# Kernel optimization log

Hardware: AMD Instinct MI355X
Metric: run time of the kernel (lower is better)

## Reference

```python
import jax, jax.numpy as jnp
import numpy as np

B, C_IN, HW, N = 128, 1024, 14, 196
D_MODEL, NH, HD, DFF = 384, 12, 32, 1536
ALPHA, BETA, GAMMA = 1.9, 3.8, 15.2
BETA_INT = int(BETA)          # 3
S = 2 * BETA_INT + 1          # 7
NUM_BUCKETS = S * S           # 49
BN_EPS = 2e-5


def _piecewise_index(d):
    # iRPE piecewise index (numpy, static): linear inside |d|<=alpha, log outside
    ad = np.abs(d).astype(np.float64)
    y = np.sign(d) * np.minimum(
        np.round(ALPHA + np.log(np.maximum(ad, ALPHA) / ALPHA) / np.log(GAMMA / ALPHA) * (BETA - ALPHA)),
        BETA)
    return np.where(ad <= ALPHA, d, y).astype(np.int64)  # trunc toward zero like torch .to(int)


def _make_rp_bucket():
    coords = np.stack(np.meshgrid(np.arange(HW), np.arange(HW), indexing='ij'), -1).reshape(-1, 2)
    diff = coords[:, None, :] - coords[None, :, :]  # [N,N,2]
    r = _piecewise_index(diff[..., 0]) + BETA_INT   # [0, 2*beta_int]
    c = _piecewise_index(diff[..., 1]) + BETA_INT
    return (r * S + c).astype(np.int32)            # [N,N] in [0,49)


RP_BUCKET = jnp.asarray(_make_rp_bucket())  # [196,196] int32, static


def _ln(x, w, b, eps=1e-5):
    mu = x.mean(-1, keepdims=True)
    var = ((x - mu) ** 2).mean(-1, keepdims=True)
    return (x - mu) * jax.lax.rsqrt(var + eps) * w + b


def setup_inputs() -> dict:
    key = jax.random.key(0)
    ks = jax.random.split(key, 12)
    g = lambda i, shape, s=0.02: jax.random.normal(ks[i], shape, jnp.float32) * s
    return {
        'x': jax.random.normal(ks[0], (B, C_IN, HW, HW), jnp.float32),
        'embed_fc1_w': g(1, (1024, C_IN)), 'embed_fc1_b': jnp.zeros((1024,), jnp.float32),
        'embed_fc2_w': g(2, (D_MODEL, 1024)), 'embed_fc2_b': jnp.zeros((D_MODEL,), jnp.float32),
        'pos_conv_w': g(3, (D_MODEL, 1, 3, 3), 0.1), 'pos_conv_b': jnp.zeros((D_MODEL,), jnp.float32),
        'ln1_w': jnp.ones((D_MODEL,), jnp.float32), 'ln1_b': jnp.zeros((D_MODEL,), jnp.float32),
        'qkv_w': g(4, (3 * D_MODEL, D_MODEL)),
        'rpe_table': g(5, (HD, NUM_BUCKETS)),
        'proj_w': g(6, (D_MODEL, D_MODEL)), 'proj_b': jnp.zeros((D_MODEL,), jnp.float32),
        'ln2_w': jnp.ones((D_MODEL,), jnp.float32), 'ln2_b': jnp.zeros((D_MODEL,), jnp.float32),
        'mlp_fc1_w': g(7, (DFF, D_MODEL)), 'mlp_fc1_b': jnp.zeros((DFF,), jnp.float32),
        'mlp_fc2_w': g(8, (D_MODEL, DFF)), 'mlp_fc2_b': jnp.zeros((D_MODEL,), jnp.float32),
        'bn1_w': jnp.ones((N,), jnp.float32), 'bn1_b': jnp.zeros((N,), jnp.float32),
        'lin_w': g(9, (D_MODEL, D_MODEL * N)), 'lin_b': jnp.zeros((D_MODEL,), jnp.float32),
        'bn2_w': jnp.ones((D_MODEL,), jnp.float32), 'bn2_b': jnp.zeros((D_MODEL,), jnp.float32),
    }


def reference(x, embed_fc1_w, embed_fc1_b, embed_fc2_w, embed_fc2_b,
              pos_conv_w, pos_conv_b, ln1_w, ln1_b, qkv_w, rpe_table,
              proj_w, proj_b, ln2_w, ln2_b, mlp_fc1_w, mlp_fc1_b,
              mlp_fc2_w, mlp_fc2_b, bn1_w, bn1_b, lin_w, lin_b, bn2_w, bn2_b):
    b = x.shape[0]
    # --- EmbedMLP: [B,C,14,14] -> [B,196,C] -> relu6 MLP -> [B,196,384]
    t = x.reshape(b, C_IN, N).transpose(0, 2, 1)
    t = jnp.clip(t @ embed_fc1_w.T + embed_fc1_b, 0.0, 6.0)
    t = t @ embed_fc2_w.T + embed_fc2_b
    # --- PosCNN: depthwise 3x3 conv + residual
    img = t.transpose(0, 2, 1).reshape(b, D_MODEL, HW, HW)
    conv = jax.lax.conv_general_dilated(
        img, pos_conv_w, (1, 1), 'SAME',
        dimension_numbers=('NCHW', 'OIHW', 'NCHW'), feature_group_count=D_MODEL)
    img = conv + pos_conv_b[None, :, None, None] + img
    t = img.reshape(b, D_MODEL, N).transpose(0, 2, 1)  # [B,196,384]
    # --- Attention with iRPE-on-k bias
    h = _ln(t, ln1_w, ln1_b)
    qkv = (h @ qkv_w.T).reshape(b, N, 3, NH, HD).transpose(2, 0, 3, 1, 4)
    scale = HD ** -0.5
    q = qkv[0] * scale
    k = qkv[1]
    v = qkv[2]
    attn = jnp.einsum('bhid,bhjd->bhij', q, k)
    # ctx-mode shared-head rpe_k: bias[b,h,i,j] = sum_d q[b,h,i,d] * table[d, bucket[i,j]]
    rpe_scores = jnp.einsum('bhid,dn->bhin', q, rpe_table)        # [B,H,N,49]
    bias = rpe_scores[:, :, jnp.arange(N)[:, None], RP_BUCKET]     # [B,H,N,N]
    attn = jax.nn.softmax(attn + bias, axis=-1)
    out = jnp.einsum('bhij,bhjd->bhid', attn, v)
    out = out.transpose(0, 2, 1, 3).reshape(b, N, D_MODEL)
    t = t + (out @ proj_w.T + proj_b)
    # --- MLP block
    h = _ln(t, ln2_w, ln2_b)
    h = jnp.clip(h @ mlp_fc1_w.T + mlp_fc1_b, 0.0, 6.0)
    t = t + (h @ mlp_fc2_w.T + mlp_fc2_b)
    # --- BatchNorm1d(196) over dims (batch, feature) per token channel (train-mode stats)
    mu = t.mean(axis=(0, 2), keepdims=True)
    var = t.var(axis=(0, 2), keepdims=True)
    t = (t - mu) * jax.lax.rsqrt(var + BN_EPS) * bn1_w[None, :, None] + bn1_b[None, :, None]
    # --- Flatten + Linear(196*384 -> 384)
    y = t.reshape(b, N * D_MODEL) @ lin_w.T + lin_b
    # --- BatchNorm1d(384) over batch (train-mode stats)
    mu2 = y.mean(axis=0, keepdims=True)
    var2 = y.var(axis=0, keepdims=True)
    y = (y - mu2) * jax.lax.rsqrt(var2 + BN_EPS) * bn2_w + bn2_b
    return y
```

## Files before the change

### kernel.cpp

```cpp
#include <hip/hip_runtime.h>
#include <cstdint>

#define B_    128
#define CIN   1024
#define NPOS  196
#define DM    384
#define NH_   12
#define HD_   32
#define DFF_  1536
#define MT    25088
#define SCALE_Q 0.17677669529663687f

typedef unsigned short u16;
typedef __attribute__((ext_vector_type(8))) short  short8;
typedef __attribute__((ext_vector_type(4))) float  f32x4;

__device__ __forceinline__ u16 f2bf(float f) {
  union { float f; uint32_t u; } v; v.f = f;
  uint32_t u = v.u;
  return (u16)((u + 0x7fffu + ((u >> 16) & 1u)) >> 16);
}
__device__ __forceinline__ float bf2f(u16 h) {
  union { uint32_t u; float f; } v; v.u = ((uint32_t)h) << 16;
  return v.f;
}

#define GLDS16(g, l)                                                           \
  __builtin_amdgcn_global_load_lds(                                            \
      (const __attribute__((address_space(1))) void*)(g),                      \
      (__attribute__((address_space(3))) void*)(l), 16, 0, 0)

template <int MODE>
__global__ __launch_bounds__(256) void gemm_k(
    const u16* __restrict__ A, const void* __restrict__ Wv,
    const float* __restrict__ bias, const float* __restrict__ res,
    void* __restrict__ outp,
    int M, int N, int K, int lda, int ldw, int nTN, int splitK)
{
  __shared__ __align__(16) u16 As[2][4 * 128 * 8];
  __shared__ __align__(16) u16 Bs[2][4 * 128 * 8];

  int nwg = gridDim.x;
  int bid0 = blockIdx.x;
  int qq = nwg >> 3, rr = nwg & 7;
  int xcd = bid0 & 7, idx = bid0 >> 3;
  int bid = (xcd < rr ? xcd * (qq + 1) : rr * (qq + 1) + (xcd - rr) * qq) + idx;

  int split = 0, mT, nT;
  if (MODE == 4) { split = bid / nTN; nT = bid % nTN; mT = 0; }
  else           { mT = bid / nTN;    nT = bid % nTN; }

  const u16* Ab = A + (size_t)split * splitK;
  float* outF = (float*)outp + ((MODE == 4) ? (size_t)split * (size_t)M * N : (size_t)0);
  u16*   outU = (u16*)outp;

  int tid = threadIdx.x;
  int wv = tid >> 6, ln = tid & 63;
  int q = ln >> 4, c = ln & 15;
  int wr = wv >> 1, wc = wv & 1;
  int mBase = mT * 128, nBase = nT * 128;

  f32x4 acc[4][4];
#pragma unroll
  for (int i = 0; i < 4; i++)
#pragma unroll
    for (int j = 0; j < 4; j++) acc[i][j] = (f32x4){0.f, 0.f, 0.f, 0.f};

  const u16* Ag = Ab + (size_t)mBase * lda;
  const u16*  Wg16 = (const u16*)Wv + (size_t)split * splitK + (size_t)nBase * ldw;
  const float* Wg32 = (const float*)Wv + (size_t)split * splitK + (size_t)nBase * ldw;

  int sl = ln & 3, rsub = ln >> 2;

  short8 ra[2], rb16[2];
  float4 rbf[2][2];

  auto LOADREG = [&](int t) {
    int k0 = t * 32;
#pragma unroll
    for (int i = 0; i < 2; i++) {
      int r = wv * 32 + i * 16 + rsub;
      ra[i] = *(const short8*)(Ag + (size_t)r * lda + k0 + sl * 8);
      if constexpr (MODE == 4) {
        const float* wp = Wg32 + (size_t)r * ldw + k0 + sl * 8;
        rbf[i][0] = *(const float4*)wp;
        rbf[i][1] = *(const float4*)(wp + 4);
      } else {
        rb16[i] = *(const short8*)(Wg16 + (size_t)r * ldw + k0 + sl * 8);
      }
    }
  };
  auto WRITE = [&](int buf) {
#pragma unroll
    for (int i = 0; i < 2; i++) {
      int r = wv * 32 + i * 16 + rsub;
      *(short8*)&As[buf][(sl * 128 + r) * 8] = ra[i];
      if constexpr (MODE == 4) {
        short8 pk;
        pk[0] = (short)f2bf(rbf[i][0].x); pk[1] = (short)f2bf(rbf[i][0].y);
        pk[2] = (short)f2bf(rbf[i][0].z); pk[3] = (short)f2bf(rbf[i][0].w);
        pk[4] = (short)f2bf(rbf[i][1].x); pk[5] = (short)f2bf(rbf[i][1].y);
        pk[6] = (short)f2bf(rbf[i][1].z); pk[7] = (short)f2bf(rbf[i][1].w);
        *(short8*)&Bs[buf][(sl * 128 + r) * 8] = pk;
      } else {
        *(short8*)&Bs[buf][(sl * 128 + r) * 8] = rb16[i];
      }
    }
  };

  int NT = K >> 5;

  LOADREG(0);
  WRITE(0);
  if (NT > 1) LOADREG(1);
  asm volatile("s_waitcnt lgkmcnt(0)" ::: "memory");
  __builtin_amdgcn_s_barrier();

  int cur = 0;
  for (int t = 0; t < NT; ++t) {
    if (t + 1 < NT) WRITE(cur ^ 1);
    short8 afr[4], bfr[4];
#pragma unroll
    for (int mt2 = 0; mt2 < 4; mt2++)
      afr[mt2] = *(const short8*)&As[cur][((q * 128) + wr * 64 + mt2 * 16 + c) * 8];
#pragma unroll
    for (int nt2 = 0; nt2 < 4; nt2++)
      bfr[nt2] = *(const short8*)&Bs[cur][((q * 128) + wc * 64 + nt2 * 16 + c) * 8];
    if (t + 2 < NT) LOADREG(t + 2);
    __builtin_amdgcn_sched_barrier(0);
#pragma unroll
    for (int mt2 = 0; mt2 < 4; mt2++)
#pragma unroll
      for (int nt2 = 0; nt2 < 4; nt2++)
        acc[mt2][nt2] = __builtin_amdgcn_mfma_f32_16x16x32_bf16(
            afr[mt2], bfr[nt2], acc[mt2][nt2], 0, 0, 0);
    asm volatile("s_waitcnt lgkmcnt(0)" ::: "memory");
    __builtin_amdgcn_s_barrier();
    cur ^= 1;
  }

#pragma unroll
  for (int mt2 = 0; mt2 < 4; mt2++) {
    int row0 = mBase + wr * 64 + mt2 * 16 + q * 4;
#pragma unroll
    for (int nt2 = 0; nt2 < 4; nt2++) {
      int col = nBase + wc * 64 + nt2 * 16 + c;
      float bv = (MODE == 0 || MODE == 1 || MODE == 3) ? bias[col] : 0.f;
      f32x4 v = acc[mt2][nt2];
#pragma unroll
      for (int e = 0; e < 4; e++) {
        int row = row0 + e;
        float x = v[e] + bv;
        if (MODE == 0) x = fminf(fmaxf(x, 0.f), 6.f);
        if (MODE == 3) x += res[(size_t)row * N + col];
        if (MODE == 0 || MODE == 2) outU[(size_t)row * N + col] = f2bf(x);
        else                        outF[(size_t)row * N + col] = x;
      }
    }
  }
}

__global__ __launch_bounds__(224) void blut_k(uint8_t* __restrict__ lut)
{
  int i = blockIdx.x;
  int j = threadIdx.x;
  uint8_t v = 49;
  if (j < 196) {
    int ri = i / 14, ci = i - ri * 14;
    int rj = j / 14, cj = j - rj * 14;
    int dr = ri - rj, dc = ci - cj;
    int adr = dr < 0 ? -dr : dr, adc = dc < 0 ? -dc : dc;
    int tr = adr <= 1 ? adr : (adr <= 3 ? 2 : 3);
    int tc = adc <= 1 ? adc : (adc <= 3 ? 2 : 3);
    int fr = dr < 0 ? -tr : tr, fc = dc < 0 ? -tc : tc;
    v = (uint8_t)(fr * 7 + fc + 24);
  }
  lut[i * 224 + j] = v;
}

__global__ __launch_bounds__(256) void attn_k(
    const u16* __restrict__ QKV, const float* __restrict__ tabG,
    const uint8_t* __restrict__ lutG, u16* __restrict__ AO)
{
  __shared__ __align__(16) u16 Ks[4 * 196 * 8];
  __shared__ __align__(16) u16 Vt[32 * 228];
  __shared__ __align__(16) u16 Pc4[4][2][512];
  __shared__ __align__(16) u16 Ts[49 * 32];
  __shared__ __align__(16) u16 Rw4[4][2][16 * 50];
  int bh = blockIdx.x; int b = bh / NH_, h = bh % NH_;
  int tid = threadIdx.x;
  int wv = tid >> 6, ln = tid & 63;
  int q = ln >> 4, c = ln & 15;
  size_t rowbase = (size_t)b * NPOS * 1152 + h * 32;

  for (int cb = wv * 64; cb < 784; cb += 256) {
    int ch = cb + ln;
    if (ch < 784) {
      int s = ch / 196, j = ch - s * 196;
      GLDS16(QKV + rowbase + 384 + (size_t)j * 1152 + s * 8, &Ks[cb * 8]);
    }
  }
  for (int t = tid; t < 49 * 32; t += 256) {
    int tt = t >> 5, k = t & 31;
    Ts[t] = f2bf(tabG[k * 49 + tt]);
  }
  for (int t = tid; t < 784; t += 256) {
    int nn = t >> 2, d0 = (t & 3) * 8;
    short8 v = *(const short8*)(QKV + rowbase + 768 + (size_t)nn * 1152 + d0);
#pragma unroll
    for (int j = 0; j < 8; j++) Vt[(d0 + j) * 228 + nn] = (u16)v[j];
  }
  for (int t = tid; t < 32 * 32; t += 256) {
    int d = t >> 5, jj = 196 + (t & 31);
    Vt[d * 228 + jj] = 0;
  }
  __syncthreads();

  for (int it = 0; it < 2; ++it) {
    int mtA = wv + it * 8;
    bool vB = (mtA + 4) < 13;
    int mbx[2];
    mbx[0] = mtA * 16;
    mbx[1] = (vB ? (mtA + 4) : 12) * 16;

    short8 afrag[2];
    int i0x[2], lutOff[2][4];
#pragma unroll
    for (int x = 0; x < 2; x++) {
      int irow = mbx[x] + c; if (irow > 195) irow = 195;
      afrag[x] = *(const short8*)(QKV + rowbase + (size_t)irow * 1152 + q * 8);
      i0x[x] = mbx[x] + q * 4;
#pragma unroll
      for (int e = 0; e < 4; e++) {
        int i = i0x[x] + e; if (i > 195) i = 195;
        lutOff[x][e] = i * 224;
      }
    }
    int rwOff[4];
#pragma unroll
    for (int e = 0; e < 4; e++) rwOff[e] = (q * 4 + e) * 50;

#pragma unroll
    for (int nt = 0; nt < 4; nt++) {
      int t = nt * 16 + c;
      int tt = t < 49 ? t : 48;
      short8 tb = *(const short8*)&Ts[tt * 32 + q * 8];
#pragma unroll
      for (int x = 0; x < 2; x++) {
        f32x4 z = {0.f, 0.f, 0.f, 0.f};
        f32x4 rr = __builtin_amdgcn_mfma_f32_16x16x32_bf16(afrag[x], tb, z, 0, 0, 0);
        if (t < 49) {
#pragma unroll
          for (int e = 0; e < 4; e++)
            Rw4[wv][x][rwOff[e] + t] = f2bf(rr[e] * SCALE_Q);
        }
      }
    }
    if (c == 0) {
#pragma unroll
      for (int x = 0; x < 2; x++)
#pragma unroll
        for (int e = 0; e < 4; e++)
          Rw4[wv][x][rwOff[e] + 49] = 0xFF80;
    }

    float mr[2] = {-INFINITY, -INFINITY};
    float l4[2][4] = {{0.f,0.f,0.f,0.f},{0.f,0.f,0.f,0.f}};
    f32x4 oacc[2][2];
#pragma unroll
    for (int x = 0; x < 2; x++) {
      oacc[x][0] = (f32x4){0.f, 0.f, 0.f, 0.f};
      oacc[x][1] = (f32x4){0.f, 0.f, 0.f, 0.f};
    }

    for (int ck = 0; ck < 7; ck++) {
      short8 bfr[2];
#pragma unroll
      for (int t = 0; t < 2; t++) {
        int j = (ck * 2 + t) * 16 + c;
        int jc = j > 195 ? 195 : j;
        bfr[t] = *(const short8*)&Ks[(q * 196 + jc) * 8];
      }
      f32x4 s01[2][2];
#pragma unroll
      for (int x = 0; x < 2; x++) {
        f32x4 z = {0.f, 0.f, 0.f, 0.f};
        s01[x][0] = __builtin_amdgcn_mfma_f32_16x16x32_bf16(afrag[x], bfr[0], z, 0, 0, 0);
        s01[x][1] = __builtin_amdgcn_mfma_f32_16x16x32_bf16(afrag[x], bfr[1], z, 0, 0, 0);
      }
      uint8_t bk[2][2][4];
#pragma unroll
      for (int t = 0; t < 2; t++) {
        int jj = ck * 32 + t * 16 + c;
#pragma unroll
        for (int x = 0; x < 2; x++)
#pragma unroll
          for (int e = 0; e < 4; e++) bk[x][t][e] = lutG[lutOff[x][e] + jj];
      }
#pragma unroll
      for (int x = 0; x < 2; x++)
#pragma unroll
        for (int t = 0; t < 2; t++)
#pragma unroll
          for (int e = 0; e < 4; e++)
            s01[x][t][e] = s01[x][t][e] * SCALE_Q + bf2f(Rw4[wv][x][rwOff[e] + bk[x][t][e]]);

#pragma unroll
      for (int x = 0; x < 2; x++) {
        float mc = s01[x][0][0];
#pragma unroll
        for (int t = 0; t < 2; t++)
#pragma unroll
          for (int e = 0; e < 4; e++) mc = fmaxf(mc, s01[x][t][e]);
#pragma unroll
        for (int o = 1; o < 16; o <<= 1) mc = fmaxf(mc, __shfl_xor(mc, o, 64));
        float mn = fmaxf(mr[x], mc);
        float sc = __expf(mr[x] - mn);
        mr[x] = mn;
#pragma unroll
        for (int t = 0; t < 2; t++)
#pragma unroll
          for (int e = 0; e < 4; e++) s01[x][t][e] = __expf(s01[x][t][e] - mn);
#pragma unroll
        for (int e = 0; e < 4; e++) {
          l4[x][e] = l4[x][e] * sc + s01[x][0][e] + s01[x][1][e];
          oacc[x][0][e] *= sc; oacc[x][1][e] *= sc;
        }
#pragma unroll
        for (int t = 0; t < 2; t++) {
          int sl2 = t * 2 + (c >> 3);
#pragma unroll
          for (int e = 0; e < 4; e++) {
            union { float f; uint32_t u; } pv; pv.f = s01[x][t][e];
            Pc4[wv][x][(sl2 * 16 + q * 4 + e) * 8 + (c & 7)] = (u16)(pv.u >> 16);
          }
        }
      }
#pragma unroll
      for (int n2 = 0; n2 < 2; n2++) {
        short8 vb = *(const short8*)&Vt[(n2 * 16 + c) * 228 + ck * 32 + q * 8];
#pragma unroll
        for (int x = 0; x < 2; x++) {
          short8 pa = *(const short8*)&Pc4[wv][x][(q * 16 + c) * 8];
          oacc[x][n2] = __builtin_amdgcn_mfma_f32_16x16x32_bf16(pa, vb, oacc[x][n2], 0, 0, 0);
        }
      }
    }

#pragma unroll
    for (int x = 0; x < 2; x++) {
      if (x == 1 && !vB) continue;
      float inv[4];
#pragma unroll
      for (int e = 0; e < 4; e++) {
        float s2 = l4[x][e];
#pragma unroll
        for (int o = 1; o < 16; o <<= 1) s2 += __shfl_xor(s2, o, 64);
        inv[e] = 1.f / s2;
      }
#pragma unroll
      for (int n2 = 0; n2 < 2; n2++) {
#pragma unroll
        for (int e = 0; e < 4; e++) {
          int i = i0x[x] + e;
          if (i < 196) {
            int d = n2 * 16 + c;
            AO[((size_t)b * NPOS + i) * DM + h * 32 + d] = f2bf(oacc[x][n2][e] * inv[e]);
          }
        }
      }
    }
  }
}

__global__ __launch_bounds__(256) void transpose_cast_k(
    const float* __restrict__ x, u16* __restrict__ At)
{
  __shared__ float t[32][33];
  int c0 = blockIdx.x * 32, n0 = blockIdx.y * 32, b = blockIdx.z;
  int tx = threadIdx.x, ty = threadIdx.y;
  const float* xb = x + (size_t)b * CIN * NPOS;
#pragma unroll
  for (int i = 0; i < 4; i++) {
    int cc = c0 + ty + i * 8, nn = n0 + tx;
    t[ty + i * 8][tx] = (nn < NPOS) ? xb[(size_t)cc * NPOS + nn] : 0.f;
  }
  __syncthreads();
  u16* Ab = At + (size_t)b * NPOS * CIN;
#pragma unroll
  for (int i = 0; i < 4; i++) {
    int nn = n0 + ty + i * 8, cc = c0 + tx;
    if (nn < NPOS) Ab[(size_t)nn * CIN + cc] = f2bf(t[tx][ty + i * 8]);
  }
}

__global__ __launch_bounds__(256) void conv_res_k(
    const float* __restrict__ T0, const float* __restrict__ pcw,
    const float* __restrict__ pcb, float* __restrict__ T1)
{
  int idx = blockIdx.x * 256 + threadIdx.x;
  if (idx >= B_ * NPOS * 96) return;
  int d4 = idx % 96; int rem = idx / 96;
  int n = rem % NPOS; int b = rem / NPOS;
  int hh = n / 14, ww = n % 14;
  int d0 = d4 * 4;
  float w9[4][9];
#pragma unroll
  for (int j = 0; j < 4; j++)
#pragma unroll
    for (int t = 0; t < 9; t++) w9[j][t] = pcw[(d0 + j) * 9 + t];
  const float* base = T0 + (size_t)b * NPOS * DM;
  float4 ctr = *(const float4*)(base + (size_t)n * DM + d0);
  float ax = ctr.x + pcb[d0], ay = ctr.y + pcb[d0 + 1];
  float az = ctr.z + pcb[d0 + 2], aw = ctr.w + pcb[d0 + 3];
#pragma unroll
  for (int kh = 0; kh < 3; kh++) {
    int h2 = hh + kh - 1;
    if (h2 < 0 || h2 >= 14) continue;
#pragma unroll
    for (int kw = 0; kw < 3; kw++) {
      int w2 = ww + kw - 1;
      if (w2 < 0 || w2 >= 14) continue;
      float4 v = *(const float4*)(base + (size_t)(h2 * 14 + w2) * DM + d0);
      int t = kh * 3 + kw;
      ax += v.x * w9[0][t]; ay += v.y * w9[1][t];
      az += v.z * w9[2][t]; aw += v.w * w9[3][t];
    }
  }
  float4 o = {ax, ay, az, aw};
  *(float4*)(T1 + (size_t)b * NPOS * DM + (size_t)n * DM + d0) = o;
}

__global__ __launch_bounds__(256) void ln_k(
    const float* __restrict__ in, const float* __restrict__ w,
    const float* __restrict__ bb, u16* __restrict__ out)
{
  int row = blockIdx.x * 4 + (threadIdx.x >> 6);
  int ln = threadIdx.x & 63;
  const float2* r = (const float2*)(in + (size_t)row * DM);
  float2 v[3]; float s = 0.f, sq = 0.f;
#pragma unroll
  for (int j = 0; j < 3; j++) {
    v[j] = r[ln + 64 * j];
    s += v[j].x + v[j].y; sq += v[j].x * v[j].x + v[j].y * v[j].y;
  }
#pragma unroll
  for (int o = 1; o < 64; o <<= 1) { s += __shfl_xor(s, o, 64); sq += __shfl_xor(sq, o, 64); }
  float mu = s * (1.f / 384.f);
  float var = sq * (1.f / 384.f) - mu * mu;
  float rs = rsqrtf(var + 1e-5f);
  uint32_t* orow = (uint32_t*)(out + (size_t)row * DM);
#pragma unroll
  for (int j = 0; j < 3; j++) {
    int d = (ln + 64 * j) * 2;
    float a = (v[j].x - mu) * rs * w[d] + bb[d];
    float bq = (v[j].y - mu) * rs * w[d + 1] + bb[d + 1];
    orow[ln + 64 * j] = (uint32_t)f2bf(a) | ((uint32_t)f2bf(bq) << 16);
  }
}

__global__ __launch_bounds__(256) void bn1_partial_k(
    const float* __restrict__ T3, float* __restrict__ part)
{
  int n = blockIdx.x >> 3, g = blockIdx.x & 7;
  int tid = threadIdx.x;
  float s = 0.f, sq = 0.f;
  for (int b2 = g * 16; b2 < g * 16 + 16; b2++) {
    const float* p = T3 + ((size_t)b2 * NPOS + n) * DM;
    for (int d = tid; d < DM; d += 256) { float v = p[d]; s += v; sq += v * v; }
  }
#pragma unroll
  for (int o = 1; o < 64; o <<= 1) { s += __shfl_xor(s, o, 64); sq += __shfl_xor(sq, o, 64); }
  __shared__ float ls[4], lq[4];
  int wv = tid >> 6, ln = tid & 63;
  if (ln == 0) { ls[wv] = s; lq[wv] = sq; }
  __syncthreads();
  if (tid == 0) {
    part[blockIdx.x * 2]     = ls[0] + ls[1] + ls[2] + ls[3];
    part[blockIdx.x * 2 + 1] = lq[0] + lq[1] + lq[2] + lq[3];
  }
}

__global__ __launch_bounds__(256) void bn1_finish_k(
    const float* __restrict__ part, const float* __restrict__ bw,
    const float* __restrict__ bbb, float* __restrict__ scaleArr,
    float* __restrict__ shiftArr)
{
  int n = threadIdx.x;
  if (n >= NPOS) return;
  float S = 0.f, Q = 0.f;
#pragma unroll
  for (int g = 0; g < 8; g++) { S += part[(n * 8 + g) * 2]; Q += part[(n * 8 + g) * 2 + 1]; }
  float mu = S / 49152.f;
  float var = Q / 49152.f - mu * mu;
  float rs = rsqrtf(var + 2e-5f);
  float sc = rs * bw[n];
  scaleArr[n] = sc;
  shiftArr[n] = bbb[n] - mu * sc;
}

__global__ __launch_bounds__(256) void bn1_apply_k(
    const float* __restrict__ T3, const float* __restrict__ scaleArr,
    const float* __restrict__ shiftArr, u16* __restrict__ outb)
{
  int idx = blockIdx.x * 256 + threadIdx.x;
  if (idx >= MT * DM / 4) return;
  int n = (idx / 96) % NPOS;
  float4 v = *(const float4*)(T3 + (size_t)idx * 4);
  float sc = scaleArr[n], sh = shiftArr[n];
  uint32_t p0 = (uint32_t)f2bf(v.x * sc + sh) | ((uint32_t)f2bf(v.y * sc + sh) << 16);
  uint32_t p1 = (uint32_t)f2bf(v.z * sc + sh) | ((uint32_t)f2bf(v.w * sc + sh) << 16);
  ((uint2*)outb)[idx] = make_uint2(p0, p1);
}

__global__ __launch_bounds__(256) void lin_reduce_k(
    const float* __restrict__ part, const float* __restrict__ lb,
    float* __restrict__ y)
{
  int idx = blockIdx.x * 256 + threadIdx.x;
  if (idx >= 128 * DM) return;
  int col = idx % DM;
  float s = lb[col];
#pragma unroll
  for (int sp = 0; sp < 49; sp++) s += part[(size_t)sp * (128 * DM) + idx];
  y[idx] = s;
}

__global__ __launch_bounds__(64) void bn2_k(
    float* __restrict__ y, const float* __restrict__ w,
    const float* __restrict__ bb)
{
  int col = blockIdx.x; int ln = threadIdx.x;
  float v0 = y[(size_t)ln * DM + col];
  float v1 = y[(size_t)(ln + 64) * DM + col];
  float s = v0 + v1, sq = v0 * v0 + v1 * v1;
#pragma unroll
  for (int o = 1; o < 64; o <<= 1) { s += __shfl_xor(s, o, 64); sq += __shfl_xor(sq, o, 64); }
  float mu = s / 128.f;
  float var = sq / 128.f - mu * mu;
  float rs = rsqrtf(var + 2e-5f);
  float sc = rs * w[col], sh = bb[col] - mu * sc;
  y[(size_t)ln * DM + col] = v0 * sc + sh;
  y[(size_t)(ln + 64) * DM + col] = v1 * sc + sh;
}

__global__ __launch_bounds__(256) void castall_k(
    const float* __restrict__ s0, u16* __restrict__ d0,
    const float* __restrict__ s1, u16* __restrict__ d1,
    const float* __restrict__ s2, u16* __restrict__ d2,
    const float* __restrict__ s3, u16* __restrict__ d3,
    const float* __restrict__ s4, u16* __restrict__ d4,
    const float* __restrict__ s5, u16* __restrict__ d5)
{
  const int b0 = 262144, b1 = b0 + 98304, b2 = b1 + 110592,
            b3 = b2 + 36864, b4 = b3 + 147456, b5 = b4 + 147456;
  int idx = blockIdx.x * 256 + threadIdx.x;
  int stride = gridDim.x * 256;
  for (; idx < b5; idx += stride) {
    const float* s; u16* d; int l;
    if      (idx < b0) { s = s0; d = d0; l = idx; }
    else if (idx < b1) { s = s1; d = d1; l = idx - b0; }
    else if (idx < b2) { s = s2; d = d2; l = idx - b1; }
    else if (idx < b3) { s = s3; d = d3; l = idx - b2; }
    else if (idx < b4) { s = s4; d = d4; l = idx - b3; }
    else               { s = s5; d = d5; l = idx - b4; }
    float4 v = *(const float4*)(s + (size_t)l * 4);
    uint32_t p0 = (uint32_t)f2bf(v.x) | ((uint32_t)f2bf(v.y) << 16);
    uint32_t p1 = (uint32_t)f2bf(v.z) | ((uint32_t)f2bf(v.w) << 16);
    ((uint2*)d)[l] = make_uint2(p0, p1);
  }
}

extern "C" void kernel_launch(void* const* d_in, const int* in_sizes, int n_in,
                              void* d_out, int out_size, void* d_ws, size_t ws_size,
                              hipStream_t stream)
{
  (void)in_sizes; (void)n_in; (void)out_size;
  const float* x    = (const float*)d_in[0];
  const float* fc1w = (const float*)d_in[1];
  const float* fc1b = (const float*)d_in[2];
  const float* fc2w = (const float*)d_in[3];
  const float* fc2b = (const float*)d_in[4];
  const float* pcw  = (const float*)d_in[5];
  const float* pcb  = (const float*)d_in[6];
  const float* ln1w = (const float*)d_in[7];
  const float* ln1b = (const float*)d_in[8];
  const float* qkvw = (const float*)d_in[9];
  const float* rpet = (const float*)d_in[10];
  const float* projw= (const float*)d_in[11];
  const float* projb= (const float*)d_in[12];
  const float* ln2w = (const float*)d_in[13];
  const float* ln2b = (const float*)d_in[14];
  const float* m1w  = (const float*)d_in[15];
  const float* m1b  = (const float*)d_in[16];
  const float* m2w  = (const float*)d_in[17];
  const float* m2b  = (const float*)d_in[18];
  const float* bn1w = (const float*)d_in[19];
  const float* bn1b = (const float*)d_in[20];
  const float* linw = (const float*)d_in[21];
  const float* linb = (const float*)d_in[22];
  const float* bn2w = (const float*)d_in[23];
  const float* bn2b = (const float*)d_in[24];
  float* y = (float*)d_out;

  const size_t RA = 0;
  const size_t RB = 77070336;
  const size_t RC = RB + 57802752;
  const size_t RD = RC + 19267584;
  const size_t RE = RD + 38535168;
  const size_t RF = RE + 38535168;
  const size_t RG = RF + 9633792;
  const size_t RS = RG + 6422528;
  const size_t NEED = RS + 2048 + 16384 + 45056;
  if (ws_size < NEED) return;

  char* ws = (char*)d_ws;
  u16*   At    = (u16*)(ws + RA);
  u16*   MLP1  = (u16*)(ws + RA);
  u16*   U     = (u16*)(ws + RB);
  u16*   QKV   = (u16*)(ws + RB);
  u16*   T3nb  = (u16*)(ws + RB);
  u16*   H     = (u16*)(ws + RC);
  u16*   AO    = (u16*)(ws + RC);
  u16*   H2    = (u16*)(ws + RC);
  float* T0    = (float*)(ws + RD);
  float* T2    = (float*)(ws + RD);
  float* T1    = (float*)(ws + RE);
  float* T3    = (float*)(ws + RE);
  float* PART  = (float*)(ws + RF);
  u16*   wb_fc1 = (u16*)(ws + RG);
  u16*   wb_fc2 = wb_fc1 + 1048576;
  u16*   wb_qkv = wb_fc2 + 393216;
  u16*   wb_proj= wb_qkv + 442368;
  u16*   wb_m1  = wb_proj + 147456;
  u16*   wb_m2  = wb_m1 + 589824;
  float* bnS   = (float*)(ws + RS);
  float* bnSh  = bnS + 196;
  float* bnP   = (float*)(ws + RS + 2048);
  uint8_t* blut = (uint8_t*)(ws + RS + 2048 + 16384);

  castall_k<<<1024, 256, 0, stream>>>(fc1w, wb_fc1, fc2w, wb_fc2, qkvw, wb_qkv,
                                      projw, wb_proj, m1w, wb_m1, m2w, wb_m2);
  blut_k<<<196, 224, 0, stream>>>(blut);

  transpose_cast_k<<<dim3(32, 7, 128), dim3(32, 8), 0, stream>>>(x, At);

  gemm_k<0><<<196 * 8, 256, 0, stream>>>(At, wb_fc1, fc1b, nullptr, U,
                                          MT, 1024, 1024, 1024, 1024, 8, 0);
  gemm_k<1><<<196 * 3, 256, 0, stream>>>(U, wb_fc2, fc2b, nullptr, T0,
                                          MT, 384, 1024, 1024, 1024, 3, 0);
  conv_res_k<<<(B_ * NPOS * 96 + 255) / 256, 256, 0, stream>>>(T0, pcw, pcb, T1);
  ln_k<<<MT / 4, 256, 0, stream>>>(T1, ln1w, ln1b, H);
  gemm_k<2><<<196 * 9, 256, 0, stream>>>(H, wb_qkv, nullptr, nullptr, QKV,
                                          MT, 1152, 384, 384, 384, 9, 0);
  attn_k<<<1536, 256, 0, stream>>>(QKV, rpet, blut, AO);
  gemm_k<3><<<196 * 3, 256, 0, stream>>>(AO, wb_proj, projb, T1, T2,
                                          MT, 384, 384, 384, 384, 3, 0);
  ln_k<<<MT / 4, 256, 0, stream>>>(T2, ln2w, ln2b, H2);
  gemm_k<0><<<196 * 12, 256, 0, stream>>>(H2, wb_m1, m1b, nullptr, MLP1,
                                           MT, 1536, 384, 384, 384, 12, 0);
  gemm_k<3><<<196 * 3, 256, 0, stream>>>(MLP1, wb_m2, m2b, T2, T3,
                                          MT, 384, 1536, 1536, 1536, 3, 0);
  bn1_partial_k<<<196 * 8, 256, 0, stream>>>(T3, bnP);
  bn1_finish_k<<<1, 256, 0, stream>>>(bnP, bn1w, bn1b, bnS, bnSh);
  bn1_apply_k<<<(MT * DM / 4 + 255) / 256, 256, 0, stream>>>(T3, bnS, bnSh, T3nb);
  gemm_k<4><<<3 * 49, 256, 0, stream>>>(T3nb, linw, nullptr, nullptr, PART,
                                         128, 384, 1536, 75264, 75264, 3, 1536);
  lin_reduce_k<<<192, 256, 0, stream>>>(PART, linb, y);
  bn2_k<<<384, 64, 0, stream>>>(y, bn2w, bn2b);
}
```

Before: 552.5 us.

## Stage GEMM tiles with direct global-to-LDS loads and XOR-swizzled row-major layout

The bf16 A and W tiles are now copied straight from global memory into LDS with global_load_lds, skipping the trip through registers. The LDS tile layout changes from k-slice-major to row-major with an XOR swizzle on the 8-element k chunk, to avoid bank conflicts. The double-buffer schedule is rebuilt around vmcnt waits so the load for tile t+2 overlaps the MFMAs on tile t. The split-K fp32-weight mode still converts W through registers but loads one tile ahead. This frees registers and VALU/LDS-write work, at the cost of more delicate wait-count synchronisation.

```diff
diff --git a/kernel.cpp b/kernel.cpp
--- a/kernel.cpp
+++ b/kernel.cpp
@@ -37,8 +37,8 @@
     void* __restrict__ outp,
     int M, int N, int K, int lda, int ldw, int nTN, int splitK)
 {
-  __shared__ __align__(16) u16 As[2][4 * 128 * 8];
-  __shared__ __align__(16) u16 Bs[2][4 * 128 * 8];
+  __shared__ __align__(16) u16 As[2][128 * 32];
+  __shared__ __align__(16) u16 Bs[2][128 * 32];
 
   int nwg = gridDim.x;
   int bid0 = blockIdx.x;
@@ -71,72 +71,106 @@
   const float* Wg32 = (const float*)Wv + (size_t)split * splitK + (size_t)nBase * ldw;
 
   int sl = ln & 3, rsub = ln >> 2;
-
-  short8 ra[2], rb16[2];
+  int lk = sl ^ ((rsub >> 1) & 3);
+
   float4 rbf[2][2];
 
-  auto LOADREG = [&](int t) {
+  auto STAGE = [&](int t, int buf) {
     int k0 = t * 32;
 #pragma unroll
     for (int i = 0; i < 2; i++) {
-      int r = wv * 32 + i * 16 + rsub;
-      ra[i] = *(const short8*)(Ag + (size_t)r * lda + k0 + sl * 8);
-      if constexpr (MODE == 4) {
-        const float* wp = Wg32 + (size_t)r * ldw + k0 + sl * 8;
-        rbf[i][0] = *(const float4*)wp;
-        rbf[i][1] = *(const float4*)(wp + 4);
-      } else {
-        rb16[i] = *(const short8*)(Wg16 + (size_t)r * ldw + k0 + sl * 8);
-      }
+      int rb = wv * 32 + i * 16;
+      GLDS16(Ag + (size_t)(rb + rsub) * lda + k0 + lk * 8, &As[buf][rb * 32]);
+      if constexpr (MODE != 4)
+        GLDS16(Wg16 + (size_t)(rb + rsub) * ldw + k0 + lk * 8, &Bs[buf][rb * 32]);
     }
   };
-  auto WRITE = [&](int buf) {
+  auto LOADW = [&](int t) {
+    int k0 = t * 32;
 #pragma unroll
     for (int i = 0; i < 2; i++) {
-      int r = wv * 32 + i * 16 + rsub;
-      *(short8*)&As[buf][(sl * 128 + r) * 8] = ra[i];
-      if constexpr (MODE == 4) {
-        short8 pk;
-        pk[0] = (short)f2bf(rbf[i][0].x); pk[1] = (short)f2bf(rbf[i][0].y);
-        pk[2] = (short)f2bf(rbf[i][0].z); pk[3] = (short)f2bf(rbf[i][0].w);
-        pk[4] = (short)f2bf(rbf[i][1].x); pk[5] = (short)f2bf(rbf[i][1].y);
-        pk[6] = (short)f2bf(rbf[i][1].z); pk[7] = (short)f2bf(rbf[i][1].w);
-        *(short8*)&Bs[buf][(sl * 128 + r) * 8] = pk;
-      } else {
-        *(short8*)&Bs[buf][(sl * 128 + r) * 8] = rb16[i];
-      }
+      const float* wp = Wg32 + (size_t)(wv * 32 + i * 16 + rsub) * ldw + k0 + sl * 8;
+      rbf[i][0] = *(const float4*)wp;
+      rbf[i][1] = *(const float4*)(wp + 4);
     }
   };
+  auto WRITEW = [&](int buf) {
+#pragma unroll
+    for (int i = 0; i < 2; i++) {
+      int rloc = wv * 32 + i * 16 + rsub;
+      short8 pk;
+      pk[0] = (short)f2bf(rbf[i][0].x); pk[1] = (short)f2bf(rbf[i][0].y);
+      pk[2] = (short)f2bf(rbf[i][0].z); pk[3] = (short)f2bf(rbf[i][0].w);
+      pk[4] = (short)f2bf(rbf[i][1].x); pk[5] = (short)f2bf(rbf[i][1].y);
+      pk[6] = (short)f2bf(rbf[i][1].z); pk[7] = (short)f2bf(rbf[i][1].w);
+      *(short8*)&Bs[buf][rloc * 32 + (sl ^ ((rsub >> 1) & 3)) * 8] = pk;
+    }
+  };
 
   int NT = K >> 5;
-
-  LOADREG(0);
-  WRITE(0);
-  if (NT > 1) LOADREG(1);
-  asm volatile("s_waitcnt lgkmcnt(0)" ::: "memory");
+  int ksw = (c >> 1) & 3;
+
+  if constexpr (MODE == 4) {
+    STAGE(0, 0);
+    LOADW(0);
+    WRITEW(0);
+    asm volatile("s_waitcnt vmcnt(0) lgkmcnt(0)" ::: "memory");
+  } else {
+    STAGE(0, 0);
+    if (NT > 1) {
+      STAGE(1, 1);
+      asm volatile("s_waitcnt vmcnt(4)" ::: "memory");
+    } else {
+      asm volatile("s_waitcnt vmcnt(0)" ::: "memory");
+    }
+  }
   __builtin_amdgcn_s_barrier();
 
   int cur = 0;
   for (int t = 0; t < NT; ++t) {
-    if (t + 1 < NT) WRITE(cur ^ 1);
     short8 afr[4], bfr[4];
 #pragma unroll
     for (int mt2 = 0; mt2 < 4; mt2++)
-      afr[mt2] = *(const short8*)&As[cur][((q * 128) + wr * 64 + mt2 * 16 + c) * 8];
+      afr[mt2] = *(const short8*)&As[cur][(wr * 64 + mt2 * 16 + c) * 32 + (q ^ ksw) * 8];
 #pragma unroll
     for (int nt2 = 0; nt2 < 4; nt2++)
-      bfr[nt2] = *(const short8*)&Bs[cur][((q * 128) + wc * 64 + nt2 * 16 + c) * 8];
-    if (t + 2 < NT) LOADREG(t + 2);
+      bfr[nt2] = *(const short8*)&Bs[cur][(wc * 64 + nt2 * 16 + c) * 32 + (q ^ ksw) * 8];
+    asm volatile("s_waitcnt lgkmcnt(0)" ::: "memory");
     __builtin_amdgcn_sched_barrier(0);
-#pragma unroll
-    for (int mt2 = 0; mt2 < 4; mt2++)
-#pragma unroll
-      for (int nt2 = 0; nt2 < 4; nt2++)
-        acc[mt2][nt2] = __builtin_amdgcn_mfma_f32_16x16x32_bf16(
-            afr[mt2], bfr[nt2], acc[mt2][nt2], 0, 0, 0);
-    asm volatile("s_waitcnt lgkmcnt(0)" ::: "memory");
     __builtin_amdgcn_s_barrier();
-    cur ^= 1;
+
+    if constexpr (MODE == 4) {
+      if (t + 1 < NT) { STAGE(t + 1, cur ^ 1); LOADW(t + 1); WRITEW(cur ^ 1); }
+      __builtin_amdgcn_sched_barrier(0);
+#pragma unroll
+      for (int mt2 = 0; mt2 < 4; mt2++)
+#pragma unroll
+        for (int nt2 = 0; nt2 < 4; nt2++)
+          acc[mt2][nt2] = __builtin_amdgcn_mfma_f32_16x16x32_bf16(
+              afr[mt2], bfr[nt2], acc[mt2][nt2], 0, 0, 0);
+      if (t + 1 < NT) {
+        asm volatile("s_waitcnt vmcnt(0) lgkmcnt(0)" ::: "memory");
+        __builtin_amdgcn_s_barrier();
+        cur ^= 1;
+      }
+    } else {
+      if (t + 2 < NT) STAGE(t + 2, cur);
+      __builtin_amdgcn_sched_barrier(0);
+#pragma unroll
+      for (int mt2 = 0; mt2 < 4; mt2++)
+#pragma unroll
+        for (int nt2 = 0; nt2 < 4; nt2++)
+          acc[mt2][nt2] = __builtin_amdgcn_mfma_f32_16x16x32_bf16(
+              afr[mt2], bfr[nt2], acc[mt2][nt2], 0, 0, 0);
+      if (t + 1 < NT) {
+        if (t + 2 < NT)
+          asm volatile("s_waitcnt vmcnt(4)" ::: "memory");
+        else
+          asm volatile("s_waitcnt vmcnt(0)" ::: "memory");
+        __builtin_amdgcn_s_barrier();
+        cur ^= 1;
+      }
+    }
   }
 
 #pragma unroll
```

Result: no change. 556.6 us (+0.7%).
